# Kernel tuning notes

Hardware: AMD Instinct MI355X
Metric: run time of the kernel (lower is better)

The kernel has to match this reference:

```python
import jax, jax.numpy as jnp
import numpy as np

MARGIN = 1.0
B, C, D = 16384, 1000, 128


def setup_inputs() -> dict:
    key = jax.random.key(0)
    k1, k2, k3 = jax.random.split(key, 3)
    features = jax.random.normal(k1, (B, D), dtype=jnp.float32)
    targets = jax.random.randint(k2, (B,), 0, C, dtype=jnp.int64)
    class_feature_vectors = jax.random.normal(k3, (C, D), dtype=jnp.float32)
    return {"features": features, "targets": targets,
            "class_feature_vectors": class_feature_vectors}


def reference(features, targets, class_feature_vectors):
    # Squared L2 distance between every sample and every class vector:
    # dist[i, j] = sum_d (features[i, d] - class_vecs[j, d])^2
    # computed via the expansion ||f||^2 + ||c||^2 - 2 f.c to avoid a [B, C, D]
    # intermediate.
    f2 = jnp.sum(features * features, axis=1)                      # [B]
    c2 = jnp.sum(class_feature_vectors * class_feature_vectors, axis=1)  # [C]
    cross = jnp.einsum('bd,cd->bc', features, class_feature_vectors)     # [B, C]
    dist = f2[:, None] + c2[None, :] - 2.0 * cross                 # [B, C]
    # Hinge term for every NEGATIVE class (j != target[i]).
    hinge = jax.nn.relu(MARGIN - dist)                             # [B, C]
    neg_mask = targets[:, None] != jnp.arange(dist.shape[1])[None, :]
    loss = jnp.sum(jnp.where(neg_mask, hinge, 0.0)) / dist.shape[0]
    return loss
```

## Files before the change

kernel.cpp:

```cpp
#include <hip/hip_runtime.h>
#include <stdint.h>

#define B_N 16384
#define C_N 1000
#define D_N 128
#define NB_TOT 64
#define MARGIN 1.0f
#define NBLK 1024

typedef __attribute__((ext_vector_type(8))) short short8;
typedef __attribute__((ext_vector_type(4))) float f32x4;

__device__ __forceinline__ short f2bf(float f) {
    union { float f; uint32_t u; } v; v.f = f;
    uint32_t u = v.u;
    return (short)((u + 0x7FFFu + ((u >> 16) & 1u)) >> 16);
}

__device__ __forceinline__ short8 cvt8(const float4& v0, const float4& v1) {
    short8 s;
    s[0] = f2bf(v0.x); s[1] = f2bf(v0.y); s[2] = f2bf(v0.z); s[3] = f2bf(v0.w);
    s[4] = f2bf(v1.x); s[5] = f2bf(v1.y); s[6] = f2bf(v1.z); s[7] = f2bf(v1.w);
    return s;
}

__global__ __launch_bounds__(64) void prep_kernel(
    const float* __restrict__ cls, short* __restrict__ bpre,
    float* __restrict__ c2p)
{
    const int nb   = blockIdx.x;
    const int lane = threadIdx.x;
    const int l15  = lane & 15;
    const int kg   = lane >> 4;
    const int col  = nb * 16 + l15;
    const bool valid = col < C_N;

    float sq = 0.f;
    #pragma unroll
    for (int kk = 0; kk < 4; ++kk) {
        float4 v0 = make_float4(0.f, 0.f, 0.f, 0.f);
        float4 v1 = make_float4(0.f, 0.f, 0.f, 0.f);
        if (valid) {
            const float* p = cls + (size_t)col * D_N + kk * 32 + kg * 8;
            v0 = *reinterpret_cast<const float4*>(p);
            v1 = *reinterpret_cast<const float4*>(p + 4);
        }
        sq += v0.x*v0.x + v0.y*v0.y + v0.z*v0.z + v0.w*v0.w
            + v1.x*v1.x + v1.y*v1.y + v1.z*v1.z + v1.w*v1.w;
        *reinterpret_cast<short8*>(bpre + (size_t)(nb * 2048 + kk * 512 + lane * 8))
            = cvt8(v0, v1);
    }
    sq += __shfl_xor(sq, 16);
    sq += __shfl_xor(sq, 32);
    if (lane < 16)
        c2p[nb * 16 + lane] = ((nb * 16 + lane) < C_N) ? sq : 1e30f;
}

__global__ __launch_bounds__(256, 4) void closs_kernel(
    const float* __restrict__ feat, const long long* __restrict__ tgt,
    const short* __restrict__ bpre, const float* __restrict__ c2p,
    float* __restrict__ part)
{
    const int tid  = threadIdx.x;
    const int wave = tid >> 6;
    const int lane = tid & 63;
    const int l15  = lane & 15;
    const int kg   = lane >> 4;

    const int bid  = blockIdx.x;
    const int xcd  = bid & 7;
    const int idx  = bid >> 3;
    const int by   = (xcd << 5) | (idx >> 2);
    const int bx   = idx & 3;
    const int row0 = by * 64 + wave * 16;
    const int nb0  = bx * 16;

    short8 a[4];
    float sq = 0.f;
    const float* ap = feat + (size_t)(row0 + l15) * D_N + kg * 8;
    #pragma unroll
    for (int kk = 0; kk < 4; ++kk) {
        float4 v0 = *reinterpret_cast<const float4*>(ap + kk * 32);
        float4 v1 = *reinterpret_cast<const float4*>(ap + kk * 32 + 4);
        sq += v0.x*v0.x + v0.y*v0.y + v0.z*v0.z + v0.w*v0.w
            + v1.x*v1.x + v1.y*v1.y + v1.z*v1.z + v1.w*v1.w;
        a[kk] = cvt8(v0, v1);
    }
    sq += __shfl_xor(sq, 16);
    sq += __shfl_xor(sq, 32);
    float t[4]; int tg[4];
    #pragma unroll
    for (int r = 0; r < 4; ++r) {
        t[r]  = MARGIN - __shfl(sq, kg * 4 + r);
        tg[r] = (int)tgt[row0 + kg * 4 + r];
    }

    float hsum = 0.f;
    #pragma unroll 4
    for (int i = 0; i < 16; ++i) {
        const int nb = nb0 + i;
        const short8* bp =
            reinterpret_cast<const short8*>(bpre + (size_t)nb * 2048) + lane;
        short8 b0 = bp[0];
        short8 b1 = bp[64];
        short8 b2 = bp[128];
        short8 b3 = bp[192];
        f32x4 acc = (f32x4){0.f, 0.f, 0.f, 0.f};
        acc = __builtin_amdgcn_mfma_f32_16x16x32_bf16(a[0], b0, acc, 0, 0, 0);
        acc = __builtin_amdgcn_mfma_f32_16x16x32_bf16(a[1], b1, acc, 0, 0, 0);
        acc = __builtin_amdgcn_mfma_f32_16x16x32_bf16(a[2], b2, acc, 0, 0, 0);
        acc = __builtin_amdgcn_mfma_f32_16x16x32_bf16(a[3], b3, acc, 0, 0, 0);

        const int   col = nb * 16 + l15;
        const float c2v = c2p[col];
        float u[4];
        float mx;
        u[0] = __builtin_fmaf(2.0f, acc[0], t[0] - c2v);
        u[1] = __builtin_fmaf(2.0f, acc[1], t[1] - c2v);
        u[2] = __builtin_fmaf(2.0f, acc[2], t[2] - c2v);
        u[3] = __builtin_fmaf(2.0f, acc[3], t[3] - c2v);
        mx = fmaxf(fmaxf(u[0], u[1]), fmaxf(u[2], u[3]));
        if (__any(mx > 0.0f)) {
            #pragma unroll
            for (int r = 0; r < 4; ++r)
                hsum += (col != tg[r]) ? fmaxf(0.0f, u[r]) : 0.0f;
        }
    }

    #pragma unroll
    for (int off = 32; off; off >>= 1) hsum += __shfl_down(hsum, off);
    __shared__ float ws[4];
    if (lane == 0) ws[wave] = hsum;
    __syncthreads();
    if (tid == 0)
        part[bid] = ws[0] + ws[1] + ws[2] + ws[3];
}

__global__ __launch_bounds__(256) void reduce_kernel(
    const float* __restrict__ part, float* __restrict__ out)
{
    const int tid = threadIdx.x;
    float s = part[tid] + part[tid + 256] + part[tid + 512] + part[tid + 768];
    #pragma unroll
    for (int off = 32; off; off >>= 1) s += __shfl_down(s, off);
    __shared__ float ws[4];
    if ((tid & 63) == 0) ws[tid >> 6] = s;
    __syncthreads();
    if (tid == 0) out[0] = (ws[0] + ws[1] + ws[2] + ws[3]) * (1.0f / 16384.0f);
}

extern "C" void kernel_launch(void* const* d_in, const int* in_sizes, int n_in,
                              void* d_out, int out_size, void* d_ws, size_t ws_size,
                              hipStream_t stream) {
    const float*     feat = (const float*)d_in[0];
    const long long* tgt  = (const long long*)d_in[1];
    const float*     cls  = (const float*)d_in[2];
    float*           out  = (float*)d_out;

    short* bpre = (short*)d_ws;
    float* c2p  = (float*)((char*)d_ws + 64 * 2048 * sizeof(short));
    float* part = c2p + 1024;

    prep_kernel<<<64, 64, 0, stream>>>(cls, bpre, c2p);
    closs_kernel<<<NBLK, 256, 0, stream>>>(feat, tgt, bpre, c2p, part);
    reduce_kernel<<<1, 256, 0, stream>>>(part, out);
}
```

Measured before the change: 24.88 us.

## Double-buffer B fragments and split MFMA accumulator chains

Prefetches the class-vector bf16 fragments two tiles ahead into register double buffers, and issues the first loads before the feature loads. It also preloads all 16 c2 values into registers and fully unrolls the loop. The four dependent MFMAs per tile become two independent accumulator chains that are summed afterward, which shortens the dependency chain. The cost is higher register pressure, which could reduce occupancy under launch_bounds(256,4).

```diff
diff --git a/kernel.cpp b/kernel.cpp
--- a/kernel.cpp
+++ b/kernel.cpp
@@ -4,7 +4,6 @@
 #define B_N 16384
 #define C_N 1000
 #define D_N 128
-#define NB_TOT 64
 #define MARGIN 1.0f
 #define NBLK 1024
 
@@ -22,6 +21,15 @@
     s[0] = f2bf(v0.x); s[1] = f2bf(v0.y); s[2] = f2bf(v0.z); s[3] = f2bf(v0.w);
     s[4] = f2bf(v1.x); s[5] = f2bf(v1.y); s[6] = f2bf(v1.z); s[7] = f2bf(v1.w);
     return s;
+}
+
+__device__ __forceinline__ void load_bfrag(const short* __restrict__ bpre,
+                                           int nb, int lane, short8* dst) {
+    const short8* bp = reinterpret_cast<const short8*>(bpre + (size_t)nb * 2048) + lane;
+    dst[0] = bp[0];
+    dst[1] = bp[64];
+    dst[2] = bp[128];
+    dst[3] = bp[192];
 }
 
 __global__ __launch_bounds__(64) void prep_kernel(
@@ -75,6 +83,14 @@
     const int row0 = by * 64 + wave * 16;
     const int nb0  = bx * 16;
 
+    short8 b0[4], b1[4];
+    load_bfrag(bpre, nb0 + 0, lane, b0);
+    load_bfrag(bpre, nb0 + 1, lane, b1);
+
+    float c2r[16];
+    #pragma unroll
+    for (int i = 0; i < 16; ++i) c2r[i] = c2p[(nb0 + i) * 16 + l15];
+
     short8 a[4];
     float sq = 0.f;
     const float* ap = feat + (size_t)(row0 + l15) * D_N + kg * 8;
@@ -96,31 +112,26 @@
     }
 
     float hsum = 0.f;
-    #pragma unroll 4
+    #pragma unroll
     for (int i = 0; i < 16; ++i) {
-        const int nb = nb0 + i;
-        const short8* bp =
-            reinterpret_cast<const short8*>(bpre + (size_t)nb * 2048) + lane;
-        short8 b0 = bp[0];
-        short8 b1 = bp[64];
-        short8 b2 = bp[128];
-        short8 b3 = bp[192];
-        f32x4 acc = (f32x4){0.f, 0.f, 0.f, 0.f};
-        acc = __builtin_amdgcn_mfma_f32_16x16x32_bf16(a[0], b0, acc, 0, 0, 0);
-        acc = __builtin_amdgcn_mfma_f32_16x16x32_bf16(a[1], b1, acc, 0, 0, 0);
-        acc = __builtin_amdgcn_mfma_f32_16x16x32_bf16(a[2], b2, acc, 0, 0, 0);
-        acc = __builtin_amdgcn_mfma_f32_16x16x32_bf16(a[3], b3, acc, 0, 0, 0);
+        short8* bc = (i & 1) ? b1 : b0;
+        f32x4 pA = (f32x4){0.f, 0.f, 0.f, 0.f};
+        f32x4 pB = (f32x4){0.f, 0.f, 0.f, 0.f};
+        pA = __builtin_amdgcn_mfma_f32_16x16x32_bf16(a[0], bc[0], pA, 0, 0, 0);
+        pB = __builtin_amdgcn_mfma_f32_16x16x32_bf16(a[1], bc[1], pB, 0, 0, 0);
+        pA = __builtin_amdgcn_mfma_f32_16x16x32_bf16(a[2], bc[2], pA, 0, 0, 0);
+        pB = __builtin_amdgcn_mfma_f32_16x16x32_bf16(a[3], bc[3], pB, 0, 0, 0);
+        if (i + 2 < 16)
+            load_bfrag(bpre, nb0 + i + 2, lane, bc);
 
-        const int   col = nb * 16 + l15;
-        const float c2v = c2p[col];
+        const float c2v = c2r[i];
         float u[4];
-        float mx;
-        u[0] = __builtin_fmaf(2.0f, acc[0], t[0] - c2v);
-        u[1] = __builtin_fmaf(2.0f, acc[1], t[1] - c2v);
-        u[2] = __builtin_fmaf(2.0f, acc[2], t[2] - c2v);
-        u[3] = __builtin_fmaf(2.0f, acc[3], t[3] - c2v);
-        mx = fmaxf(fmaxf(u[0], u[1]), fmaxf(u[2], u[3]));
+        #pragma unroll
+        for (int r = 0; r < 4; ++r)
+            u[r] = __builtin_fmaf(2.0f, pA[r] + pB[r], t[r] - c2v);
+        const float mx = fmaxf(fmaxf(u[0], u[1]), fmaxf(u[2], u[3]));
         if (__any(mx > 0.0f)) {
+            const int col = (nb0 + i) * 16 + l15;
             #pragma unroll
             for (int r = 0; r < 4; ++r)
                 hsum += (col != tg[r]) ? fmaxf(0.0f, u[r]) : 0.0f;
```

Measured after the change: 24.30 us. -2.4%, faster.
